# Kernel tuning notes

Measured on AMD Instinct MI355X. Metric: run time of the kernel, lower is better.

The kernel has to match this reference:

```python
import jax, jax.numpy as jnp
import numpy as np

DIM = 2048
N_HEADS = 16
N_KV_HEADS = 8
HEAD_DIM = DIM // N_HEADS  # 128
B, S = 4, 2048
EPS = 1e-6


def _xavier_uniform(key, shape):
    fan_out, fan_in = shape
    bound = float(np.sqrt(6.0 / (fan_in + fan_out)))
    return jax.random.uniform(key, shape, jnp.float32, -bound, bound)


def _rmsnorm(x, w):
    # x: [..., head_dim]
    return x * jax.lax.rsqrt(jnp.mean(x * x, axis=-1, keepdims=True) + EPS) * w


def _apply_rope(x, cos, sin):
    # x: [B,S,H,D]; cos/sin: [B,S,D//2]; pairs (even, odd) form complex numbers
    x2 = x.reshape(*x.shape[:-1], HEAD_DIM // 2, 2)
    xr, xi = x2[..., 0], x2[..., 1]
    c = cos[:, :, None, :]
    s = sin[:, :, None, :]
    out_r = xr * c - xi * s
    out_i = xr * s + xi * c
    return jnp.stack([out_r, out_i], axis=-1).reshape(x.shape)


def setup_inputs() -> dict:
    key = jax.random.key(0)
    k1, k2, k3 = jax.random.split(key, 3)
    x = jax.random.normal(k1, (B, S, DIM), jnp.float32)
    x_mask = jnp.ones((B, S), jnp.bool_)
    # rotary frequencies (llama-style)
    inv_freq = 1.0 / (10000.0 ** (np.arange(0, HEAD_DIM, 2, dtype=np.float32) / HEAD_DIM))
    angles = np.arange(S, dtype=np.float32)[:, None] * inv_freq[None, :]  # [S, D/2]
    freqs_cos = jnp.broadcast_to(jnp.asarray(np.cos(angles)), (B, S, HEAD_DIM // 2))
    freqs_sin = jnp.broadcast_to(jnp.asarray(np.sin(angles)), (B, S, HEAD_DIM // 2))
    qkv_out = (N_HEADS + 2 * N_KV_HEADS) * HEAD_DIM
    Wqkv = _xavier_uniform(k2, (qkv_out, DIM))
    Wout = _xavier_uniform(k3, (DIM, N_HEADS * HEAD_DIM))
    qn_w = jnp.ones((HEAD_DIM,), jnp.float32)
    kn_w = jnp.ones((HEAD_DIM,), jnp.float32)
    return {"x": x, "x_mask": x_mask, "freqs_cos": freqs_cos, "freqs_sin": freqs_sin,
            "Wqkv": Wqkv, "Wout": Wout, "qn_w": qn_w, "kn_w": kn_w}


def reference(x, x_mask, freqs_cos, freqs_sin, Wqkv, Wout, qn_w, kn_w):
    bsz, seqlen, _ = x.shape
    n_rep = N_HEADS // N_KV_HEADS
    qkv = x @ Wqkv.T  # [B,S,(H+2*KV)*D]
    q_sz = N_HEADS * HEAD_DIM
    kv_sz = N_KV_HEADS * HEAD_DIM
    xq = qkv[..., :q_sz].reshape(bsz, seqlen, N_HEADS, HEAD_DIM)
    xk = qkv[..., q_sz:q_sz + kv_sz].reshape(bsz, seqlen, N_KV_HEADS, HEAD_DIM)
    xv = qkv[..., q_sz + kv_sz:].reshape(bsz, seqlen, N_KV_HEADS, HEAD_DIM)
    xq = _rmsnorm(xq, qn_w)
    xk = _rmsnorm(xk, kn_w)
    xq = _apply_rope(xq, freqs_cos, freqs_sin)
    xk = _apply_rope(xk, freqs_cos, freqs_sin)
    # GQA: repeat kv heads contiguously (matches unsqueeze(3).repeat.flatten(2,3))
    xk = jnp.repeat(xk, n_rep, axis=2)  # [B,S,H,D]
    xv = jnp.repeat(xv, n_rep, axis=2)
    scale = float(np.sqrt(1.0 / HEAD_DIM))
    scores = jnp.einsum('bqhd,bkhd->bhqk', xq, xk) * scale  # [B,H,S,S]
    mask = x_mask[:, None, None, :]  # [B,1,1,S] key mask
    scores = jnp.where(mask, scores, jnp.asarray(-1e30, scores.dtype))
    attn = jax.nn.softmax(scores, axis=-1)
    out = jnp.einsum('bhqk,bkhd->bqhd', attn, xv)  # [B,S,H,D]
    out = out.reshape(bsz, seqlen, N_HEADS * HEAD_DIM)
    return out @ Wout.T
```

## Files before the change

kernel.cpp:

```cpp
#include <hip/hip_runtime.h>

typedef unsigned short u16;
typedef unsigned int   u32;
typedef __bf16  bf16x8 __attribute__((ext_vector_type(8)));
typedef float   f32x4  __attribute__((ext_vector_type(4)));
typedef u16     u16x8  __attribute__((ext_vector_type(8)));
typedef u32     u32x4  __attribute__((ext_vector_type(4)));

#define DEV __device__ __forceinline__

DEV u16 f2bf(float f) {
  u32 u = __builtin_bit_cast(u32, f);
  u += 0x7fffu + ((u >> 16) & 1u);
  return (u16)(u >> 16);
}
DEV float bf2f(u16 h) { return __builtin_bit_cast(float, (u32)h << 16); }

DEV void gl2lds16(const void* g, void* l) {
  __builtin_amdgcn_global_load_lds(
      (const __attribute__((address_space(1))) u32*)g,
      (__attribute__((address_space(3))) u32*)l, 16, 0, 0);
}

DEV f32x4 mfma16(u16x8 a, u16x8 b, f32x4 c) {
  return __builtin_amdgcn_mfma_f32_16x16x32_bf16(
      __builtin_bit_cast(bf16x8, a), __builtin_bit_cast(bf16x8, b), c, 0, 0, 0);
}

DEV u32 cvtpk(float lo, float hi) {
  u32 d;
  asm("v_cvt_pk_bf16_f32 %0, %1, %2" : "=v"(d) : "v"(lo), "v"(hi));
  return d;
}
DEV void pl32swap(u32 &a, u32 &b) {
  asm("v_permlane32_swap_b32 %0, %1" : "+v"(a), "+v"(b));
}
DEV void pl16swap(u32 &a, u32 &b) {
  asm("v_permlane16_swap_b32 %0, %1" : "+v"(a), "+v"(b));
}

__global__ __launch_bounds__(256) void k_cast3(
    const float* __restrict__ x, const float* __restrict__ wq,
    const float* __restrict__ wo, u16* __restrict__ out)
{
  long e = ((long)blockIdx.x * 256 + threadIdx.x) * 8;
  if (e >= 29360128L) return;
  const float* src;
  long off;
  if (e < 16777216L)      { src = x;  off = e; }
  else if (e < 25165824L) { src = wq; off = e - 16777216L; }
  else                    { src = wo; off = e - 25165824L; }
  float4 a = *(const float4*)(src + off);
  float4 b = *(const float4*)(src + off + 4);
  u16x8 o;
  o[0]=f2bf(a.x); o[1]=f2bf(a.y); o[2]=f2bf(a.z); o[3]=f2bf(a.w);
  o[4]=f2bf(b.x); o[5]=f2bf(b.y); o[6]=f2bf(b.z); o[7]=f2bf(b.w);
  *(u16x8*)(out + e) = o;
}

template<bool F32OUT>
__global__ __launch_bounds__(512, 2) void k_gemm256(
    const u16* __restrict__ A, const u16* __restrict__ B,
    u16* __restrict__ Cb, float* __restrict__ Cf, int N, int K, int nbx)
{
  __shared__ __align__(16) u16 As2[2][16384];
  __shared__ __align__(16) u16 Bs2[2][16384];

  const int per = gridDim.x >> 3;
  const int wg  = (blockIdx.x & 7) * per + (blockIdx.x >> 3);
  const int by  = wg / nbx, bx = wg - by * nbx;
  const long m0 = (long)by * 256, n0 = (long)bx * 256;

  const int tid = threadIdx.x, wv = tid >> 6, lane = tid & 63;
  const int lr = lane & 15, lg = lane >> 4;
  const int wr = wv >> 2, wc = wv & 3;

  const int r8  = tid >> 3;
  const int u   = tid & 7;
  const int kux = ((u ^ (r8 & 7)) << 3);

  const int aoffb = wr * 8192 + lr * 64;
  const int boffb = (wc >> 1) * 8192 + (wc & 1) * 4096 + lr * 64;
  const int sw0 = ((lg ^ (lr & 7)) << 3);
  const int sw1 = (((4 + lg) ^ (lr & 7)) << 3);

  f32x4 acc[8][4] = {};

  auto stA = [&](int d, int k0, int h, int rh) {
    gl2lds16(A + (m0 + h * 128 + rh * 64 + r8) * (long)K + k0 + kux,
             &As2[d][h * 8192 + rh * 4096 + tid * 8]);
  };
  auto stB = [&](int d, int k0, int h, int rh) {
    gl2lds16(B + (n0 + h * 128 + rh * 64 + r8) * (long)K + k0 + kux,
             &Bs2[d][h * 8192 + rh * 4096 + tid * 8]);
  };

  const int T = K >> 6;
#pragma unroll
  for (int h = 0; h < 2; ++h)
#pragma unroll
    for (int rh = 0; rh < 2; ++rh) { stA(0, 0, h, rh); stB(0, 0, h, rh); }
  if (T > 1) {
    stB(1, 64, 0, 0); stB(1, 64, 0, 1); stB(1, 64, 1, 0); stB(1, 64, 1, 1);
    stA(1, 64, 0, 0); stA(1, 64, 1, 0);
  }

  for (int t = 0; t < T; ++t) {
    const int d = t & 1;
    if (t < T - 1) asm volatile("s_waitcnt vmcnt(6)" ::: "memory");
    else           asm volatile("s_waitcnt vmcnt(0)" ::: "memory");
    asm volatile("s_barrier" ::: "memory");

    u16x8 bfrag[4][2], afrag[2][2];
#pragma unroll
    for (int g = 0; g < 4; ++g) {
      bfrag[g][0] = *(const u16x8*)(&Bs2[d][boffb + g * 1024 + sw0]);
      bfrag[g][1] = *(const u16x8*)(&Bs2[d][boffb + g * 1024 + sw1]);
    }
#pragma unroll
    for (int j = 0; j < 2; ++j) {
      afrag[j][0] = *(const u16x8*)(&As2[d][aoffb + j * 1024 + sw0]);
      afrag[j][1] = *(const u16x8*)(&As2[d][aoffb + j * 1024 + sw1]);
    }
    if (t + 1 < T) {
      stA(d ^ 1, (t + 1) << 6, 0, 1);
      stA(d ^ 1, (t + 1) << 6, 1, 1);
    }
    asm volatile("s_barrier" ::: "memory");
    __builtin_amdgcn_s_setprio(1);
#pragma unroll
    for (int j = 0; j < 2; ++j)
#pragma unroll
      for (int g = 0; g < 4; ++g)
#pragma unroll
        for (int kk = 0; kk < 2; ++kk)
          acc[j][g] = mfma16(afrag[j][kk], bfrag[g][kk], acc[j][g]);
    __builtin_amdgcn_s_setprio(0);

#pragma unroll
    for (int p = 1; p < 4; ++p) {
      const int f0 = 2 * p;
#pragma unroll
      for (int j = 0; j < 2; ++j) {
        afrag[j][0] = *(const u16x8*)(&As2[d][aoffb + (f0 + j) * 1024 + sw0]);
        afrag[j][1] = *(const u16x8*)(&As2[d][aoffb + (f0 + j) * 1024 + sw1]);
      }
      if (t + 2 < T) {
        const int k2 = (t + 2) << 6;
        if (p == 1) { stB(d, k2, 0, 0); stB(d, k2, 0, 1); }
        if (p == 2) { stB(d, k2, 1, 0); stB(d, k2, 1, 1); }
        if (p == 3) { stA(d, k2, 0, 0); stA(d, k2, 1, 0); }
      }
      asm volatile("s_barrier" ::: "memory");
      __builtin_amdgcn_s_setprio(1);
#pragma unroll
      for (int j = 0; j < 2; ++j)
#pragma unroll
        for (int g = 0; g < 4; ++g)
#pragma unroll
          for (int kk = 0; kk < 2; ++kk)
            acc[f0 + j][g] = mfma16(afrag[j][kk], bfrag[g][kk], acc[f0 + j][g]);
      __builtin_amdgcn_s_setprio(0);
    }
  }

#pragma unroll
  for (int f = 0; f < 8; ++f)
#pragma unroll
    for (int g = 0; g < 4; ++g)
#pragma unroll
      for (int r = 0; r < 4; ++r) {
        long row = m0 + wr * 128 + f * 16 + lg * 4 + r;
        long col = n0 + wc * 64 + g * 16 + lr;
        if (F32OUT) Cf[row * N + col] = acc[f][g][r];
        else        Cb[row * N + col] = f2bf(acc[f][g][r]);
      }
}

__global__ __launch_bounds__(384) void k_normrope(
    const u16* __restrict__ qkv, const float* __restrict__ fc,
    const float* __restrict__ fs, const float* __restrict__ qn,
    const float* __restrict__ kn,
    u16* __restrict__ Qg, u16* __restrict__ Kg)
{
  const int m = blockIdx.x;
  const int b = m >> 11, s = m & 2047;
  const int wave = threadIdx.x >> 6, lane = threadIdx.x & 63;
  const int sub = lane >> 4;
  const int l16 = lane & 15;
  const int slot = wave * 4 + sub;
  const int d0 = l16 * 8;
  const float QS = 0.12751744f;

  u16x8 v = *(const u16x8*)(qkv + (long)m * 4096 + slot * 128 + d0);
  float xv[8];
#pragma unroll
  for (int j = 0; j < 8; ++j) xv[j] = bf2f(v[j]);

  float ss = 0.f;
#pragma unroll
  for (int j = 0; j < 8; ++j) ss += xv[j] * xv[j];
#pragma unroll
  for (int msk = 1; msk < 16; msk <<= 1) ss += __shfl_xor(ss, msk, 64);
  float rms = rsqrtf(ss * (1.0f / 128.0f) + 1e-6f);

  const bool isq = slot < 16;
  const float* wp = (isq ? qn : kn) + d0;
  float4 wa = *(const float4*)(wp);
  float4 wb = *(const float4*)(wp + 4);
  float w[8] = {wa.x, wa.y, wa.z, wa.w, wb.x, wb.y, wb.z, wb.w};

  float4 ca = *(const float4*)(fc + (long)m * 64 + l16 * 4);
  float4 sa = *(const float4*)(fs + (long)m * 64 + l16 * 4);
  float cc[4] = {ca.x, ca.y, ca.z, ca.w};
  float sn[4] = {sa.x, sa.y, sa.z, sa.w};

  u16x8 o;
#pragma unroll
  for (int p = 0; p < 4; ++p) {
    float xr = xv[2 * p]     * rms * w[2 * p];
    float xi = xv[2 * p + 1] * rms * w[2 * p + 1];
    float o0 = xr * cc[p] - xi * sn[p];
    float o1 = xr * sn[p] + xi * cc[p];
    if (isq) { o0 *= QS; o1 *= QS; }
    o[2 * p]     = f2bf(o0);
    o[2 * p + 1] = f2bf(o1);
  }
  if (isq)
    *(u16x8*)(Qg + ((long)((b * 16 + slot) * 2048 + s)) * 128 + d0) = o;
  else
    *(u16x8*)(Kg + ((long)((b * 8 + slot - 16) * 2048 + s)) * 128 + d0) = o;
}

__global__ __launch_bounds__(256) void k_vtrans(const u16* __restrict__ qkv,
                                                u16* __restrict__ Vt)
{
  __shared__ __align__(16) u16 Ls[128 * 128];
  const int st = blockIdx.x;
  const int bk = blockIdx.y;
  const int b = bk >> 3, kvh = bk & 7;
  const int t = threadIdx.x;
  const int s0 = st * 128;
  const u16* src = qkv + ((long)(b * 2048 + s0)) * 4096 + (24 + kvh) * 128;
#pragma unroll
  for (int i = 0; i < 8; ++i) {
    int gi = i * 2048 + t * 8;
    int sl = gi >> 7, d = gi & 127;
    u16x8 v = *(const u16x8*)(src + (long)sl * 4096 + d);
    int sw = ((sl ^ (sl >> 3)) & 7) << 3;
    *(u16x8*)(&Ls[sl * 128 + (d ^ sw)]) = v;
  }
  __syncthreads();
  u16* dst = Vt + ((long)bk * 128) * 2048 + s0;
#pragma unroll
  for (int i = 0; i < 8; ++i) {
    int d = i * 16 + (t >> 4);
    int sl0 = (t & 15) * 8;
    u16x8 o;
#pragma unroll
    for (int j = 0; j < 8; ++j) {
      int sl = sl0 + j;
      int sw = ((sl ^ (sl >> 3)) & 7) << 3;
      o[j] = Ls[sl * 128 + (d ^ sw)];
    }
    *(u16x8*)(dst + (long)d * 2048 + sl0) = o;
  }
}

__global__ __launch_bounds__(512, 4) void k_attn(
    const u16* __restrict__ Qg, const u16* __restrict__ Kg,
    const u16* __restrict__ Vt, u16* __restrict__ Og)
{
  __shared__ __align__(16) u16 Kl[2 * 64 * 128];
  __shared__ __align__(16) u16 Vl[2 * 128 * 64];

  const int f   = blockIdx.x;
  const int xcd = f & 7;
  const int s7  = f >> 3;
  const int b   = s7 >> 5;
  const int kvh = xcd;
  const int mem = s7 & 31;
  const int h   = kvh * 2 + (mem & 1);
  const int qblk= mem >> 1;

  const u16*  Qp = Qg + (long)(b * 16 + h) * 2048 * 128;
  const char* Kp = (const char*)(Kg + (long)(b * 8 + kvh) * 2048 * 128);
  const char* Vp = (const char*)(Vt + (long)(b * 8 + kvh) * 128 * 2048);

  const int tid = threadIdx.x, wave = tid >> 6, lane = tid & 63;
  const int lr = lane & 15, lg = lane >> 4;
  const int q0 = qblk * 128 + wave * 16;

  u16x8 qf[4];
#pragma unroll
  for (int kk = 0; kk < 4; ++kk)
    qf[kk] = *(const u16x8*)(Qp + (long)(q0 + lr) * 128 + kk * 32 + lg * 8);

  u16x8 ones;
#pragma unroll
  for (int j = 0; j < 8; ++j) ones[j] = 0x3F80;

  f32x4 oacc[8] = {};
  f32x4 lacc = {};

  int koff[2], voff[2];
#pragma unroll
  for (int i = 0; i < 2; ++i) {
    int L = i * 8192 + tid * 16;
    int key = L >> 8;
    koff[i] = key * 256 + ((L & 255) ^ ((key & 7) << 4));
    int d = L >> 7;
    voff[i] = d * 4096 + ((L & 127) ^ ((d & 7) << 4));
  }
  char* Klb = (char*)Kl;
  char* Vlb = (char*)Vl;

  auto stage = [&](int sel, int k0) {
#pragma unroll
    for (int i = 0; i < 2; ++i) {
      int L = i * 8192 + tid * 16;
      gl2lds16(Kp + (long)k0 * 256 + koff[i], Klb + sel * 16384 + L);
      gl2lds16(Vp + (long)k0 * 2   + voff[i], Vlb + sel * 16384 + L);
    }
  };

  stage(0, 0);

  int cur = 0;
  for (int t = 0; t < 32; ++t) {
    if (t < 31) {
      stage(cur ^ 1, (t + 1) * 64);
      asm volatile("s_waitcnt vmcnt(4)" ::: "memory");
    } else {
      asm volatile("s_waitcnt vmcnt(0)" ::: "memory");
    }
    asm volatile("s_barrier" ::: "memory");
    const u16* Kb = Kl + cur * 8192;
    const u16* Vb = Vl + cur * 8192;

#pragma unroll
    for (int h32 = 0; h32 < 2; ++h32) {
      f32x4 sf[2] = {};
      __builtin_amdgcn_s_setprio(1);
#pragma unroll
      for (int kk = 0; kk < 4; ++kk)
#pragma unroll
        for (int nt = 0; nt < 2; ++nt) {
          const int krow = h32 * 32 + nt * 16 + lr;
          u16x8 kf = *(const u16x8*)(&Kb[krow * 128 +
                                         ((kk * 32 + lg * 8) ^ ((krow & 7) << 3))]);
          sf[nt] = mfma16(kf, qf[kk], sf[nt]);
        }
      __builtin_amdgcn_s_setprio(0);

      float e[2][4];
#pragma unroll
      for (int nt = 0; nt < 2; ++nt)
#pragma unroll
        for (int r = 0; r < 4; ++r) e[nt][r] = exp2f(sf[nt][r]);
      u32 w00 = cvtpk(e[0][0], e[0][1]), w01 = cvtpk(e[0][2], e[0][3]);
      u32 w10 = cvtpk(e[1][0], e[1][1]), w11 = cvtpk(e[1][2], e[1][3]);
      pl32swap(w00, w10);  pl32swap(w01, w11);
      pl16swap(w00, w10);  pl16swap(w01, w11);
      u32x4 pu = {w00, w01, w10, w11};
      u16x8 pav = __builtin_bit_cast(u16x8, pu);

      __builtin_amdgcn_s_setprio(1);
#pragma unroll
      for (int n = 0; n < 8; ++n) {
        u16x8 vb = *(const u16x8*)(&Vb[(n * 16 + lr) * 64 +
                                       ((h32 * 32 + lg * 8) ^ ((lr & 7) << 3))]);
        oacc[n] = mfma16(pav, vb, oacc[n]);
      }
      lacc = mfma16(pav, ones, lacc);
      __builtin_amdgcn_s_setprio(0);
    }

    asm volatile("s_barrier" ::: "memory");
    cur ^= 1;
  }

  float inv[4];
#pragma unroll
  for (int r = 0; r < 4; ++r) inv[r] = 1.0f / lacc[r];

  const long sbase = (long)b * 2048 + q0;
#pragma unroll
  for (int n = 0; n < 8; ++n)
#pragma unroll
    for (int r = 0; r < 4; ++r) {
      long srow = sbase + lg * 4 + r;
      Og[srow * 2048 + h * 128 + n * 16 + lr] = f2bf(oacc[n][r] * inv[r]);
    }
}

extern "C" void kernel_launch(void* const* d_in, const int* in_sizes, int n_in,
                              void* d_out, int out_size, void* d_ws, size_t ws_size,
                              hipStream_t stream) {
  const float* x    = (const float*)d_in[0];
  const float* fc   = (const float*)d_in[2];
  const float* fs   = (const float*)d_in[3];
  const float* Wqkv = (const float*)d_in[4];
  const float* Wout = (const float*)d_in[5];
  const float* qn   = (const float*)d_in[6];
  const float* kn   = (const float*)d_in[7];
  float* out = (float*)d_out;

  const size_t XB_OFF   = 0;
  const size_t WQKV_OFF = 33554432;
  const size_t WOUT_OFF = 50331648;
  const size_t QKV_OFF  = 58720256;
  const size_t KG_OFF   = 125829120;
  const size_t VT_OFF   = 142606336;
  if (ws_size < 159383552) return;

  char* ws = (char*)d_ws;
  u16* castb = (u16*)(ws + XB_OFF);
  u16* xb    = (u16*)(ws + XB_OFF);
  u16* wqkvb = (u16*)(ws + WQKV_OFF);
  u16* woutb = (u16*)(ws + WOUT_OFF);
  u16* qkvb  = (u16*)(ws + QKV_OFF);
  u16* Qgb   = (u16*)(ws + XB_OFF);
  u16* Kgb   = (u16*)(ws + KG_OFF);
  u16* Vtb   = (u16*)(ws + VT_OFF);
  u16* Ogb   = (u16*)(ws + QKV_OFF);

  k_cast3<<<14336, 256, 0, stream>>>(x, Wqkv, Wout, castb);

  k_gemm256<false><<<512, 512, 0, stream>>>(xb, wqkvb, qkvb, nullptr, 4096, 2048, 16);

  k_vtrans<<<dim3(16, 32), 256, 0, stream>>>(qkvb, Vtb);
  k_normrope<<<8192, 384, 0, stream>>>(qkvb, fc, fs, qn, kn, Qgb, Kgb);

  k_attn<<<1024, 512, 0, stream>>>(Qgb, Kgb, Vtb, Ogb);

  k_gemm256<true><<<256, 512, 0, stream>>>(Ogb, woutb, nullptr, out, 2048, 2048, 8);
}
```

Before: 404.7 us.

## Fuse QK RMSNorm and RoPE into QKV GEMM epilogue, read Q/K in place

Adds a specialized QKV GEMM whose epilogue, for Q and K column blocks, computes per-head RMS across waves through LDS, applies the norm weight, RoPE (pairing lanes via shuffle) and the Q scale, then writes back into the qkv buffer. This removes the separate normrope kernel and its extra read/write pass. Attention now reads Q and K directly from the interleaved qkv layout with a 4096-element row stride instead of from compact per-head buffers. The strided Q/K loads may coalesce worse, and the epilogue does scattered cos/sin loads plus extra shuffles and register pressure.

Measured after the change: 409.2 us. Within noise of the previous version (+1.1%).

```diff
diff --git a/kernel.cpp b/kernel.cpp
--- a/kernel.cpp
+++ b/kernel.cpp
@@ -177,59 +177,181 @@
       }
 }
 
-__global__ __launch_bounds__(384) void k_normrope(
-    const u16* __restrict__ qkv, const float* __restrict__ fc,
+__global__ __launch_bounds__(512, 2) void k_gemm_qkv(
+    const u16* __restrict__ A, const u16* __restrict__ B,
+    u16* __restrict__ qkv, const float* __restrict__ fc,
     const float* __restrict__ fs, const float* __restrict__ qn,
-    const float* __restrict__ kn,
-    u16* __restrict__ Qg, u16* __restrict__ Kg)
+    const float* __restrict__ kn, int N, int K, int nbx)
 {
-  const int m = blockIdx.x;
-  const int b = m >> 11, s = m & 2047;
-  const int wave = threadIdx.x >> 6, lane = threadIdx.x & 63;
-  const int sub = lane >> 4;
-  const int l16 = lane & 15;
-  const int slot = wave * 4 + sub;
-  const int d0 = l16 * 8;
-  const float QS = 0.12751744f;
-
-  u16x8 v = *(const u16x8*)(qkv + (long)m * 4096 + slot * 128 + d0);
-  float xv[8];
-#pragma unroll
-  for (int j = 0; j < 8; ++j) xv[j] = bf2f(v[j]);
-
-  float ss = 0.f;
-#pragma unroll
-  for (int j = 0; j < 8; ++j) ss += xv[j] * xv[j];
-#pragma unroll
-  for (int msk = 1; msk < 16; msk <<= 1) ss += __shfl_xor(ss, msk, 64);
-  float rms = rsqrtf(ss * (1.0f / 128.0f) + 1e-6f);
-
-  const bool isq = slot < 16;
-  const float* wp = (isq ? qn : kn) + d0;
-  float4 wa = *(const float4*)(wp);
-  float4 wb = *(const float4*)(wp + 4);
-  float w[8] = {wa.x, wa.y, wa.z, wa.w, wb.x, wb.y, wb.z, wb.w};
-
-  float4 ca = *(const float4*)(fc + (long)m * 64 + l16 * 4);
-  float4 sa = *(const float4*)(fs + (long)m * 64 + l16 * 4);
-  float cc[4] = {ca.x, ca.y, ca.z, ca.w};
-  float sn[4] = {sa.x, sa.y, sa.z, sa.w};
-
-  u16x8 o;
-#pragma unroll
-  for (int p = 0; p < 4; ++p) {
-    float xr = xv[2 * p]     * rms * w[2 * p];
-    float xi = xv[2 * p + 1] * rms * w[2 * p + 1];
-    float o0 = xr * cc[p] - xi * sn[p];
-    float o1 = xr * sn[p] + xi * cc[p];
-    if (isq) { o0 *= QS; o1 *= QS; }
-    o[2 * p]     = f2bf(o0);
-    o[2 * p + 1] = f2bf(o1);
-  }
-  if (isq)
-    *(u16x8*)(Qg + ((long)((b * 16 + slot) * 2048 + s)) * 128 + d0) = o;
-  else
-    *(u16x8*)(Kg + ((long)((b * 8 + slot - 16) * 2048 + s)) * 128 + d0) = o;
+  __shared__ __align__(16) u16 As2[2][16384];
+  __shared__ __align__(16) u16 Bs2[2][16384];
+
+  const int per = gridDim.x >> 3;
+  const int wg  = (blockIdx.x & 7) * per + (blockIdx.x >> 3);
+  const int by  = wg / nbx, bx = wg - by * nbx;
+  const long m0 = (long)by * 256, n0 = (long)bx * 256;
+
+  const int tid = threadIdx.x, wv = tid >> 6, lane = tid & 63;
+  const int lr = lane & 15, lg = lane >> 4;
+  const int wr = wv >> 2, wc = wv & 3;
+
+  const int r8  = tid >> 3;
+  const int u   = tid & 7;
+  const int kux = ((u ^ (r8 & 7)) << 3);
+
+  const int aoffb = wr * 8192 + lr * 64;
+  const int boffb = (wc >> 1) * 8192 + (wc & 1) * 4096 + lr * 64;
+  const int sw0 = ((lg ^ (lr & 7)) << 3);
+  const int sw1 = (((4 + lg) ^ (lr & 7)) << 3);
+
+  f32x4 acc[8][4] = {};
+
+  auto stA = [&](int d, int k0, int h, int rh) {
+    gl2lds16(A + (m0 + h * 128 + rh * 64 + r8) * (long)K + k0 + kux,
+             &As2[d][h * 8192 + rh * 4096 + tid * 8]);
+  };
+  auto stB = [&](int d, int k0, int h, int rh) {
+    gl2lds16(B + (n0 + h * 128 + rh * 64 + r8) * (long)K + k0 + kux,
+             &Bs2[d][h * 8192 + rh * 4096 + tid * 8]);
+  };
+
+  const int T = K >> 6;
+#pragma unroll
+  for (int h = 0; h < 2; ++h)
+#pragma unroll
+    for (int rh = 0; rh < 2; ++rh) { stA(0, 0, h, rh); stB(0, 0, h, rh); }
+  if (T > 1) {
+    stB(1, 64, 0, 0); stB(1, 64, 0, 1); stB(1, 64, 1, 0); stB(1, 64, 1, 1);
+    stA(1, 64, 0, 0); stA(1, 64, 1, 0);
+  }
+
+  for (int t = 0; t < T; ++t) {
+    const int d = t & 1;
+    if (t < T - 1) asm volatile("s_waitcnt vmcnt(6)" ::: "memory");
+    else           asm volatile("s_waitcnt vmcnt(0)" ::: "memory");
+    asm volatile("s_barrier" ::: "memory");
+
+    u16x8 bfrag[4][2], afrag[2][2];
+#pragma unroll
+    for (int g = 0; g < 4; ++g) {
+      bfrag[g][0] = *(const u16x8*)(&Bs2[d][boffb + g * 1024 + sw0]);
+      bfrag[g][1] = *(const u16x8*)(&Bs2[d][boffb + g * 1024 + sw1]);
+    }
+#pragma unroll
+    for (int j = 0; j < 2; ++j) {
+      afrag[j][0] = *(const u16x8*)(&As2[d][aoffb + j * 1024 + sw0]);
+      afrag[j][1] = *(const u16x8*)(&As2[d][aoffb + j * 1024 + sw1]);
+    }
+    if (t + 1 < T) {
+      stA(d ^ 1, (t + 1) << 6, 0, 1);
+      stA(d ^ 1, (t + 1) << 6, 1, 1);
+    }
+    asm volatile("s_barrier" ::: "memory");
+    __builtin_amdgcn_s_setprio(1);
+#pragma unroll
+    for (int j = 0; j < 2; ++j)
+#pragma unroll
+      for (int g = 0; g < 4; ++g)
+#pragma unroll
+        for (int kk = 0; kk < 2; ++kk)
+          acc[j][g] = mfma16(afrag[j][kk], bfrag[g][kk], acc[j][g]);
+    __builtin_amdgcn_s_setprio(0);
+
+#pragma unroll
+    for (int p = 1; p < 4; ++p) {
+      const int f0 = 2 * p;
+#pragma unroll
+      for (int j = 0; j < 2; ++j) {
+        afrag[j][0] = *(const u16x8*)(&As2[d][aoffb + (f0 + j) * 1024 + sw0]);
+        afrag[j][1] = *(const u16x8*)(&As2[d][aoffb + (f0 + j) * 1024 + sw1]);
+      }
+      if (t + 2 < T) {
+        const int k2 = (t + 2) << 6;
+        if (p == 1) { stB(d, k2, 0, 0); stB(d, k2, 0, 1); }
+        if (p == 2) { stB(d, k2, 1, 0); stB(d, k2, 1, 1); }
+        if (p == 3) { stA(d, k2, 0, 0); stA(d, k2, 1, 0); }
+      }
+      asm volatile("s_barrier" ::: "memory");
+      __builtin_amdgcn_s_setprio(1);
+#pragma unroll
+      for (int j = 0; j < 2; ++j)
+#pragma unroll
+        for (int g = 0; g < 4; ++g)
+#pragma unroll
+          for (int kk = 0; kk < 2; ++kk)
+            acc[f0 + j][g] = mfma16(afrag[j][kk], bfrag[g][kk], acc[f0 + j][g]);
+      __builtin_amdgcn_s_setprio(0);
+    }
+  }
+
+  const int c0 = wc * 64;
+  if (bx >= 12) {
+#pragma unroll
+    for (int f = 0; f < 8; ++f)
+#pragma unroll
+      for (int g = 0; g < 4; ++g)
+#pragma unroll
+        for (int r = 0; r < 4; ++r) {
+          long row = m0 + wr * 128 + f * 16 + lg * 4 + r;
+          long col = n0 + c0 + g * 16 + lr;
+          qkv[row * N + col] = f2bf(acc[f][g][r]);
+        }
+    return;
+  }
+
+  asm volatile("s_waitcnt lgkmcnt(0)" ::: "memory");
+  asm volatile("s_barrier" ::: "memory");
+  float* Pl = (float*)&As2[0][0];
+
+  float tot[8][4];
+#pragma unroll
+  for (int f = 0; f < 8; ++f)
+#pragma unroll
+    for (int r = 0; r < 4; ++r) {
+      float s2 = 0.f;
+#pragma unroll
+      for (int g = 0; g < 4; ++g) s2 += acc[f][g][r] * acc[f][g][r];
+#pragma unroll
+      for (int msk = 1; msk < 16; msk <<= 1) s2 += __shfl_xor(s2, msk, 64);
+      tot[f][r] = s2;
+    }
+  if (lr == 0) {
+#pragma unroll
+    for (int f = 0; f < 8; ++f)
+#pragma unroll
+      for (int r = 0; r < 4; ++r)
+        Pl[wv * 128 + f * 16 + lg * 4 + r] = tot[f][r];
+  }
+  asm volatile("s_waitcnt lgkmcnt(0)" ::: "memory");
+  asm volatile("s_barrier" ::: "memory");
+
+  const bool isQ = (bx < 8);
+  const float* wt = isQ ? qn : kn;
+  const float QS = isQ ? 0.12751744f : 1.0f;
+  int dv[4]; float w4[4];
+#pragma unroll
+  for (int g = 0; g < 4; ++g) {
+    dv[g] = (int)((n0 + c0 + g * 16 + lr) & 127);
+    w4[g] = wt[dv[g]];
+  }
+#pragma unroll
+  for (int f = 0; f < 8; ++f)
+#pragma unroll
+    for (int r = 0; r < 4; ++r) {
+      long tok = m0 + wr * 128 + f * 16 + lg * 4 + r;
+      float t2 = tot[f][r] + Pl[(wv ^ 1) * 128 + f * 16 + lg * 4 + r];
+      float rms = rsqrtf(t2 * (1.0f / 128.0f) + 1e-6f);
+#pragma unroll
+      for (int g = 0; g < 4; ++g) {
+        float vs = acc[f][g][r] * rms * w4[g];
+        float ot = __shfl_xor(vs, 1, 64);
+        int dd = dv[g];
+        float co = fc[tok * 64 + (dd >> 1)];
+        float si = fs[tok * 64 + (dd >> 1)];
+        float o = (dd & 1) ? (ot * si + vs * co) : (vs * co - ot * si);
+        qkv[tok * N + n0 + c0 + g * 16 + lr] = f2bf(o * QS);
+      }
+    }
 }
 
 __global__ __launch_bounds__(256) void k_vtrans(const u16* __restrict__ qkv,
@@ -268,8 +390,8 @@
 }
 
 __global__ __launch_bounds__(512, 4) void k_attn(
-    const u16* __restrict__ Qg, const u16* __restrict__ Kg,
-    const u16* __restrict__ Vt, u16* __restrict__ Og)
+    const u16* __restrict__ qkv, const u16* __restrict__ Vt,
+    u16* __restrict__ Og)
 {
   __shared__ __align__(16) u16 Kl[2 * 64 * 128];
   __shared__ __align__(16) u16 Vl[2 * 128 * 64];
@@ -283,8 +405,8 @@
   const int h   = kvh * 2 + (mem & 1);
   const int qblk= mem >> 1;
 
-  const u16*  Qp = Qg + (long)(b * 16 + h) * 2048 * 128;
-  const char* Kp = (const char*)(Kg + (long)(b * 8 + kvh) * 2048 * 128);
+  const u16*  Qp = qkv + (long)b * 2048 * 4096 + h * 128;
+  const char* Kp = (const char*)(qkv + (long)b * 2048 * 4096 + 2048 + kvh * 128);
   const char* Vp = (const char*)(Vt + (long)(b * 8 + kvh) * 128 * 2048);
 
   const int tid = threadIdx.x, wave = tid >> 6, lane = tid & 63;
@@ -294,7 +416,7 @@
   u16x8 qf[4];
 #pragma unroll
   for (int kk = 0; kk < 4; ++kk)
-    qf[kk] = *(const u16x8*)(Qp + (long)(q0 + lr) * 128 + kk * 32 + lg * 8);
+    qf[kk] = *(const u16x8*)(Qp + (long)(q0 + lr) * 4096 + kk * 32 + lg * 8);
 
   u16x8 ones;
 #pragma unroll
@@ -308,7 +430,7 @@
   for (int i = 0; i < 2; ++i) {
     int L = i * 8192 + tid * 16;
     int key = L >> 8;
-    koff[i] = key * 256 + ((L & 255) ^ ((key & 7) << 4));
+    koff[i] = key * 8192 + ((L & 255) ^ ((key & 7) << 4));
     int d = L >> 7;
     voff[i] = d * 4096 + ((L & 127) ^ ((d & 7) << 4));
   }
@@ -319,8 +441,8 @@
 #pragma unroll
     for (int i = 0; i < 2; ++i) {
       int L = i * 8192 + tid * 16;
-      gl2lds16(Kp + (long)k0 * 256 + koff[i], Klb + sel * 16384 + L);
-      gl2lds16(Vp + (long)k0 * 2   + voff[i], Vlb + sel * 16384 + L);
+      gl2lds16(Kp + (long)k0 * 8192 + koff[i], Klb + sel * 16384 + L);
+      gl2lds16(Vp + (long)k0 * 2    + voff[i], Vlb + sel * 16384 + L);
     }
   };
 
@@ -410,7 +532,6 @@
   const size_t WQKV_OFF = 33554432;
   const size_t WOUT_OFF = 50331648;
   const size_t QKV_OFF  = 58720256;
-  const size_t KG_OFF   = 125829120;
   const size_t VT_OFF   = 142606336;
   if (ws_size < 159383552) return;
 
@@ -420,19 +541,17 @@
   u16* wqkvb = (u16*)(ws + WQKV_OFF);
   u16* woutb = (u16*)(ws + WOUT_OFF);
   u16* qkvb  = (u16*)(ws + QKV_OFF);
-  u16* Qgb   = (u16*)(ws + XB_OFF);
-  u16* Kgb   = (u16*)(ws + KG_OFF);
   u16* Vtb   = (u16*)(ws + VT_OFF);
-  u16* Ogb   = (u16*)(ws + QKV_OFF);
+  u16* Ogb   = (u16*)(ws + XB_OFF);
 
   k_cast3<<<14336, 256, 0, stream>>>(x, Wqkv, Wout, castb);
 
-  k_gemm256<false><<<512, 512, 0, stream>>>(xb, wqkvb, qkvb, nullptr, 4096, 2048, 16);
+  k_gemm_qkv<<<512, 512, 0, stream>>>(xb, wqkvb, qkvb, fc, fs, qn, kn,
+                                      4096, 2048, 16);
 
   k_vtrans<<<dim3(16, 32), 256, 0, stream>>>(qkvb, Vtb);
-  k_normrope<<<8192, 384, 0, stream>>>(qkvb, fc, fs, qn, kn, Qgb, Kgb);
-
-  k_attn<<<1024, 512, 0, stream>>>(Qgb, Kgb, Vtb, Ogb);
+
+  k_attn<<<1024, 512, 0, stream>>>(qkvb, Vtb, Ogb);
 
   k_gemm256<true><<<256, 512, 0, stream>>>(Ogb, woutb, nullptr, out, 2048, 2048, 8);
 }
```
